# Performance work log

Hardware: AMD Instinct MI355X
Metric: run time of the kernel (lower is better)

Reference implementation:

```python
import jax, jax.numpy as jnp
import numpy as np

B, S, D, H = 4096, 200, 64, 36
BN_EPS = 1e-5
DICE_EPS = 1e-3


def setup_inputs() -> dict:
    key = jax.random.key(0)
    ks = jax.random.split(key, 6)
    return {
        "history": jax.random.normal(ks[0], (B, S, D), dtype=jnp.float32),
        "candidate": jax.random.normal(ks[1], (B, D), dtype=jnp.float32),
        "W1": jax.random.normal(ks[2], (4 * D, H), dtype=jnp.float32) * 0.05,
        "b1": jax.random.normal(ks[3], (H,), dtype=jnp.float32) * 0.05,
        "gamma": jnp.ones((H,), dtype=jnp.float32),
        "beta": jnp.zeros((H,), dtype=jnp.float32),
        "alpha": jax.random.normal(ks[4], (1,), dtype=jnp.float32),
        "W2": jax.random.normal(ks[5], (H, 1), dtype=jnp.float32) * 0.05,
        "b2": jnp.zeros((1,), dtype=jnp.float32),
    }


def reference(history, candidate, W1, b1, gamma, beta, alpha, W2, b2):
    b, s, d = history.shape
    cand = jnp.broadcast_to(candidate[:, None, :], (b, s, d))
    att_in = jnp.concatenate([cand, history, cand - history, cand * history], axis=-1)
    x = att_in.reshape(b * s, 4 * d)
    # Linear
    h = x @ W1 + b1
    # BatchNorm1d (training mode: batch statistics, biased variance)
    mu = h.mean(axis=0)
    var = h.var(axis=0)
    h = (h - mu) * jax.lax.rsqrt(var + BN_EPS) * gamma + beta
    # Dice: per-row normalization over features, eps=1e-3
    avg = h.mean(axis=1, keepdims=True)
    v = jnp.sum((h - avg) ** 2, axis=1, keepdims=True) / h.shape[1]
    ps = jax.nn.sigmoid((h - avg) / jnp.sqrt(v + DICE_EPS))
    h = ps * h + (1.0 - ps) * alpha * h
    # Output linear -> attention weight per (b, s)
    w = (h @ W2 + b2).reshape(b, s)
    # Weighted sum pooling over sequence
    return jnp.einsum("bs,bsd->bd", w, history)
```

## Files before the change

kernel.cpp:

```cpp
#include <hip/hip_runtime.h>
#include <math.h>

#define BB 4096
#define SS 200
#define DD 64
#define HH 36
#define NP 48
#define NROWS (BB * SS)
#define LDH 72
#define MT 13

typedef short bf16x8 __attribute__((ext_vector_type(8)));
typedef float f32x4 __attribute__((ext_vector_type(4)));

__device__ __forceinline__ unsigned short f2bf(float f) {
    union { float f; unsigned u; } v; v.f = f;
    unsigned r = v.u + 0x7FFFu + ((v.u >> 16) & 1u);
    return (unsigned short)(r >> 16);
}

__device__ __forceinline__ void build_tiles(int b, int t,
                                            const float* __restrict__ hist,
                                            const float* __restrict__ cand,
                                            const float* __restrict__ W1,
                                            const float* __restrict__ b1,
                                            unsigned short* shH, unsigned short* shWbT,
                                            float* shC, float* shBase,
                                            float (*shBaseP)[NP]) {
    if (t < DD) shC[t] = cand[b * DD + t];
    for (int i = t; i < 8 * DD; i += 256) {
        int s = SS + (i >> 6), d = i & 63;
        shH[s * LDH + d] = 0;
    }
    __syncthreads();
    const float4* src = (const float4*)(hist + (size_t)b * (SS * DD));
    for (int i = t; i < SS * DD / 4; i += 256) {
        float4 v = src[i];
        int s = i >> 4, c = i & 15;
        ushort4 o;
        o.x = f2bf(v.x); o.y = f2bf(v.y); o.z = f2bf(v.z); o.w = f2bf(v.w);
        *(ushort4*)&shH[s * LDH + c * 4] = o;
    }
    for (int e = t; e < NP * DD; e += 256) {
        int k = e / NP, n = e - k * NP;
        float v = 0.f;
        if (n < HH)
            v = W1[(DD + k) * HH + n] - W1[(2 * DD + k) * HH + n] +
                shC[k] * W1[(3 * DD + k) * HH + n];
        shWbT[n * LDH + k] = f2bf(v);
    }
    if (t < 4 * NP) {
        int g = t / NP, j = t - g * NP;
        float p = 0.f;
        if (j < HH) {
#pragma unroll 4
            for (int k = 16 * g; k < 16 * g + 16; ++k)
                p += shC[k] * (W1[k * HH + j] + W1[(2 * DD + k) * HH + j]);
        }
        shBaseP[g][j] = p;
    }
    __syncthreads();
    if (t < NP) {
        float v = (t < HH) ? b1[t] : 0.f;
        shBase[t] = v + shBaseP[0][t] + shBaseP[1][t] + shBaseP[2][t] + shBaseP[3][t];
    }
    __syncthreads();
}

__device__ __forceinline__ void load_bfrags(const unsigned short* shWbT, int lane,
                                            bf16x8 (&bfr)[3][2]) {
    int col = lane & 15, q = lane >> 4;
#pragma unroll
    for (int nt = 0; nt < 3; ++nt)
#pragma unroll
        for (int kt = 0; kt < 2; ++kt)
            bfr[nt][kt] = *(const bf16x8*)&shWbT[(nt * 16 + col) * LDH + kt * 32 + q * 8];
}

__device__ __forceinline__ void gemm_tile(const unsigned short* shH,
                                          const bf16x8 (&bfr)[3][2], int mt, int lane,
                                          f32x4 (&d)[3]) {
    int m = mt * 16 + (lane & 15), q = lane >> 4;
    d[0] = f32x4{0.f, 0.f, 0.f, 0.f};
    d[1] = f32x4{0.f, 0.f, 0.f, 0.f};
    d[2] = f32x4{0.f, 0.f, 0.f, 0.f};
#pragma unroll
    for (int kt = 0; kt < 2; ++kt) {
        bf16x8 a = *(const bf16x8*)&shH[m * LDH + kt * 32 + q * 8];
#pragma unroll
        for (int nt = 0; nt < 3; ++nt)
            d[nt] = __builtin_amdgcn_mfma_f32_16x16x32_bf16(a, bfr[nt][kt], d[nt], 0, 0, 0);
    }
}

__global__ __launch_bounds__(256, 4) void k_pass1(const float* __restrict__ hist,
                                                  const float* __restrict__ cand,
                                                  const float* __restrict__ W1,
                                                  const float* __restrict__ b1,
                                                  float* __restrict__ gsum,
                                                  float* __restrict__ gsum2) {
    __shared__ unsigned short shH[208 * LDH];
    __shared__ unsigned short shWbT[NP * LDH];
    __shared__ float shC[DD], shBase[NP];
    __shared__ float shBaseP[4][NP];
    __shared__ float shP1[4][NP], shP2[4][NP];
    int b = blockIdx.x, t = threadIdx.x, wave = t >> 6, lane = t & 63;
    int col = lane & 15, q = lane >> 4;

    build_tiles(b, t, hist, cand, W1, b1, shH, shWbT, shC, shBase, shBaseP);

    bf16x8 bfr[3][2];
    load_bfrags(shWbT, lane, bfr);
    float basev[3];
#pragma unroll
    for (int nt = 0; nt < 3; ++nt) basev[nt] = shBase[nt * 16 + col];

    float cs1[3] = {0.f, 0.f, 0.f}, cs2[3] = {0.f, 0.f, 0.f};
    for (int mt = wave; mt < MT; mt += 4) {
        f32x4 d[3];
        gemm_tile(shH, bfr, mt, lane, d);
        int row0 = mt * 16 + q * 4;
#pragma unroll
        for (int nt = 0; nt < 3; ++nt)
#pragma unroll
            for (int r = 0; r < 4; ++r) {
                if (row0 + r < SS) {
                    float v = d[nt][r] + basev[nt];
                    cs1[nt] += v;
                    cs2[nt] += v * v;
                }
            }
    }
#pragma unroll
    for (int nt = 0; nt < 3; ++nt) {
        cs1[nt] += __shfl_xor(cs1[nt], 16);
        cs1[nt] += __shfl_xor(cs1[nt], 32);
        cs2[nt] += __shfl_xor(cs2[nt], 16);
        cs2[nt] += __shfl_xor(cs2[nt], 32);
    }
    if (lane < 16) {
#pragma unroll
        for (int nt = 0; nt < 3; ++nt) {
            shP1[wave][nt * 16 + lane] = cs1[nt];
            shP2[wave][nt * 16 + lane] = cs2[nt];
        }
    }
    __syncthreads();
    if (t < HH) {
        atomicAdd(gsum + t, shP1[0][t] + shP1[1][t] + shP1[2][t] + shP1[3][t]);
        atomicAdd(gsum2 + t, shP2[0][t] + shP2[1][t] + shP2[2][t] + shP2[3][t]);
    }
}

__global__ void k_stats(const float* __restrict__ gsum, const float* __restrict__ gsum2,
                        const float* __restrict__ gamma, const float* __restrict__ beta,
                        float* __restrict__ A, float* __restrict__ Bc) {
    int t = threadIdx.x;
    if (t < NP) {
        if (t < HH) {
            float mu = gsum[t] * (1.0f / (float)NROWS);
            float var = gsum2[t] * (1.0f / (float)NROWS) - mu * mu;
            float rs = rsqrtf(var + 1e-5f);
            float a = rs * gamma[t];
            A[t] = a;
            Bc[t] = beta[t] - mu * a;
        } else {
            A[t] = 0.f;
            Bc[t] = 0.f;
        }
    }
}

__global__ __launch_bounds__(256, 4) void k_pass2(const float* __restrict__ hist,
                                                  const float* __restrict__ cand,
                                                  const float* __restrict__ W1,
                                                  const float* __restrict__ b1,
                                                  const float* __restrict__ Acoef,
                                                  const float* __restrict__ Bcoef,
                                                  const float* __restrict__ alpha,
                                                  const float* __restrict__ W2,
                                                  const float* __restrict__ b2,
                                                  float* __restrict__ out) {
    __shared__ unsigned short shH[208 * LDH];
    __shared__ unsigned short shWbT[NP * LDH];
    __shared__ float shC[DD], shBase[NP];
    __shared__ float shBaseP[4][NP];
    __shared__ float shW[208];
    __shared__ float shPool[4][DD];
    int b = blockIdx.x, t = threadIdx.x, wave = t >> 6, lane = t & 63;
    int col = lane & 15, q = lane >> 4;

    build_tiles(b, t, hist, cand, W1, b1, shH, shWbT, shC, shBase, shBaseP);

    bf16x8 bfr[3][2];
    load_bfrags(shWbT, lane, bfr);
    float basev[3], Ar[3], Br[3], W2r[3];
#pragma unroll
    for (int nt = 0; nt < 3; ++nt) {
        int c = nt * 16 + col;
        basev[nt] = shBase[c];
        Ar[nt] = Acoef[c];
        Br[nt] = Bcoef[c];
        W2r[nt] = (c < HH) ? W2[c] : 0.f;
    }
    float alv = alpha[0], b2v = b2[0];

    for (int mt = wave; mt < MT; mt += 4) {
        f32x4 d[3];
        gemm_tile(shH, bfr, mt, lane, d);
        float hp[3][4];
#pragma unroll
        for (int nt = 0; nt < 3; ++nt)
#pragma unroll
            for (int r = 0; r < 4; ++r)
                hp[nt][r] = fmaf(d[nt][r] + basev[nt], Ar[nt], Br[nt]);
        float s1[4], s2[4], wsum[4];
#pragma unroll
        for (int r = 0; r < 4; ++r) {
            s1[r] = hp[0][r] + hp[1][r] + hp[2][r];
            s2[r] = hp[0][r] * hp[0][r] + hp[1][r] * hp[1][r] + hp[2][r] * hp[2][r];
            s1[r] += __shfl_xor(s1[r], 1);
            s1[r] += __shfl_xor(s1[r], 2);
            s1[r] += __shfl_xor(s1[r], 4);
            s1[r] += __shfl_xor(s1[r], 8);
            s2[r] += __shfl_xor(s2[r], 1);
            s2[r] += __shfl_xor(s2[r], 2);
            s2[r] += __shfl_xor(s2[r], 4);
            s2[r] += __shfl_xor(s2[r], 8);
        }
#pragma unroll
        for (int r = 0; r < 4; ++r) {
            float avg = s1[r] * (1.0f / (float)HH);
            float var = s2[r] * (1.0f / (float)HH) - avg * avg;
            float inv = rsqrtf(var + 1e-3f);
            float wv = 0.f;
#pragma unroll
            for (int nt = 0; nt < 3; ++nt) {
                float z = (hp[nt][r] - avg) * inv;
                float ps = 1.0f / (1.0f + __expf(-z));
                float f = ps + (1.0f - ps) * alv;
                wv = fmaf(hp[nt][r] * f, W2r[nt], wv);
            }
            wsum[r] = wv;
            wsum[r] += __shfl_xor(wsum[r], 1);
            wsum[r] += __shfl_xor(wsum[r], 2);
            wsum[r] += __shfl_xor(wsum[r], 4);
            wsum[r] += __shfl_xor(wsum[r], 8);
        }
        if (col == 0 && !(mt == MT - 1 && q >= 2)) {
            float4 o = {wsum[0] + b2v, wsum[1] + b2v, wsum[2] + b2v, wsum[3] + b2v};
            *(float4*)&shW[mt * 16 + q * 4] = o;
        }
    }
    __syncthreads();
    {
        const float* hb = hist + (size_t)b * SS * DD;
        float p = 0.f;
        int s0 = wave * 50;
        for (int s = s0; s < s0 + 50; ++s) p = fmaf(shW[s], hb[(size_t)s * DD + lane], p);
        shPool[wave][lane] = p;
    }
    __syncthreads();
    if (t < DD)
        out[b * DD + t] = shPool[0][t] + shPool[1][t] + shPool[2][t] + shPool[3][t];
}

extern "C" void kernel_launch(void* const* d_in, const int* in_sizes, int n_in,
                              void* d_out, int out_size, void* d_ws, size_t ws_size,
                              hipStream_t stream) {
    const float* hist = (const float*)d_in[0];
    const float* cand = (const float*)d_in[1];
    const float* W1 = (const float*)d_in[2];
    const float* b1 = (const float*)d_in[3];
    const float* gamma = (const float*)d_in[4];
    const float* beta = (const float*)d_in[5];
    const float* alpha = (const float*)d_in[6];
    const float* W2 = (const float*)d_in[7];
    const float* b2 = (const float*)d_in[8];
    float* out = (float*)d_out;
    float* ws = (float*)d_ws;

    float* gsum = ws;
    float* gsum2 = ws + NP;
    float* A = ws + 2 * NP;
    float* Bc = ws + 3 * NP;

    hipMemsetAsync(gsum, 0, 2 * NP * sizeof(float), stream);
    k_pass1<<<BB, 256, 0, stream>>>(hist, cand, W1, b1, gsum, gsum2);
    k_stats<<<1, 64, 0, stream>>>(gsum, gsum2, gamma, beta, A, Bc);
    k_pass2<<<BB, 256, 0, stream>>>(hist, cand, W1, b1, A, Bc, alpha, W2, b2, out);
}
```

Baseline: 475.4 us.

## Split each batch row across two blocks with smaller LDS tiles

Each batch element is now handled by two blocks, one for rows 0-111 and one for rows 112-199, which doubles the grid and roughly halves the shared-memory footprint per block. Launch bounds rise to 6 blocks per CU and the LDS stride shrinks to 68. History loads are issued into registers before the first barrier so more memory traffic is in flight. Pooled outputs are combined with atomicAdd after a memset of the output buffer. In exchange, the candidate and weight prologue is computed twice per batch row, and the new atomics and memset add their own cost.

Result: slower. 591.5 us (+24.4%).

```diff
diff --git a/kernel.cpp b/kernel.cpp
--- a/kernel.cpp
+++ b/kernel.cpp
@@ -6,9 +6,8 @@
 #define DD 64
 #define HH 36
 #define NP 48
-#define NROWS (BB * SS)
-#define LDH 72
-#define MT 13
+#define LDH 68
+#define NROWSF (4096.0f * 200.0f)
 
 typedef short bf16x8 __attribute__((ext_vector_type(8)));
 typedef float f32x4 __attribute__((ext_vector_type(4)));
@@ -19,35 +18,46 @@
     return (unsigned short)(r >> 16);
 }
 
-__device__ __forceinline__ void build_tiles(int b, int t,
-                                            const float* __restrict__ hist,
-                                            const float* __restrict__ cand,
-                                            const float* __restrict__ W1,
-                                            const float* __restrict__ b1,
-                                            unsigned short* shH, unsigned short* shWbT,
-                                            float* shC, float* shBase,
-                                            float (*shBaseP)[NP]) {
+__device__ __forceinline__ void prologue(int b, int half, int t,
+                                         const float* __restrict__ hist,
+                                         const float* __restrict__ cand,
+                                         const float* __restrict__ W1,
+                                         const float* __restrict__ b1,
+                                         unsigned short* shH, unsigned short* shWbT,
+                                         float* shC, float* shBase,
+                                         float (*shBaseP)[NP]) {
+    const int rowLo = half ? 112 : 0;
+    const int nflt4 = half ? (88 * 16) : (112 * 16);
+    float4 v[7];
+    const float4* src = (const float4*)(hist + ((size_t)b * SS + rowLo) * DD);
+#pragma unroll
+    for (int u = 0; u < 7; ++u) {
+        int i = t + u * 256;
+        if (i < nflt4) v[u] = src[i];
+    }
     if (t < DD) shC[t] = cand[b * DD + t];
-    for (int i = t; i < 8 * DD; i += 256) {
-        int s = SS + (i >> 6), d = i & 63;
-        shH[s * LDH + d] = 0;
-    }
-    __syncthreads();
-    const float4* src = (const float4*)(hist + (size_t)b * (SS * DD));
-    for (int i = t; i < SS * DD / 4; i += 256) {
-        float4 v = src[i];
-        int s = i >> 4, c = i & 15;
-        ushort4 o;
-        o.x = f2bf(v.x); o.y = f2bf(v.y); o.z = f2bf(v.z); o.w = f2bf(v.w);
-        *(ushort4*)&shH[s * LDH + c * 4] = o;
+    if (half) {
+        for (int i = t; i < 8 * DD; i += 256)
+            shH[(88 + (i >> 6)) * LDH + (i & 63)] = 0;
+    }
+    __syncthreads();
+#pragma unroll
+    for (int u = 0; u < 7; ++u) {
+        int i = t + u * 256;
+        if (i < nflt4) {
+            int s = i >> 4, c = i & 15;
+            ushort4 o;
+            o.x = f2bf(v[u].x); o.y = f2bf(v[u].y); o.z = f2bf(v[u].z); o.w = f2bf(v[u].w);
+            *(ushort4*)&shH[s * LDH + c * 4] = o;
+        }
     }
     for (int e = t; e < NP * DD; e += 256) {
         int k = e / NP, n = e - k * NP;
-        float v = 0.f;
+        float val = 0.f;
         if (n < HH)
-            v = W1[(DD + k) * HH + n] - W1[(2 * DD + k) * HH + n] +
-                shC[k] * W1[(3 * DD + k) * HH + n];
-        shWbT[n * LDH + k] = f2bf(v);
+            val = W1[(DD + k) * HH + n] - W1[(2 * DD + k) * HH + n] +
+                  shC[k] * W1[(3 * DD + k) * HH + n];
+        shWbT[n * LDH + k] = f2bf(val);
     }
     if (t < 4 * NP) {
         int g = t / NP, j = t - g * NP;
@@ -61,8 +71,8 @@
     }
     __syncthreads();
     if (t < NP) {
-        float v = (t < HH) ? b1[t] : 0.f;
-        shBase[t] = v + shBaseP[0][t] + shBaseP[1][t] + shBaseP[2][t] + shBaseP[3][t];
+        float val = (t < HH) ? b1[t] : 0.f;
+        shBase[t] = val + shBaseP[0][t] + shBaseP[1][t] + shBaseP[2][t] + shBaseP[3][t];
     }
     __syncthreads();
 }
@@ -93,21 +103,22 @@
     }
 }
 
-__global__ __launch_bounds__(256, 4) void k_pass1(const float* __restrict__ hist,
+__global__ __launch_bounds__(256, 6) void k_pass1(const float* __restrict__ hist,
                                                   const float* __restrict__ cand,
                                                   const float* __restrict__ W1,
                                                   const float* __restrict__ b1,
                                                   float* __restrict__ gsum,
                                                   float* __restrict__ gsum2) {
-    __shared__ unsigned short shH[208 * LDH];
+    __shared__ unsigned short shH[112 * LDH];
     __shared__ unsigned short shWbT[NP * LDH];
     __shared__ float shC[DD], shBase[NP];
     __shared__ float shBaseP[4][NP];
     __shared__ float shP1[4][NP], shP2[4][NP];
-    int b = blockIdx.x, t = threadIdx.x, wave = t >> 6, lane = t & 63;
+    int bx = blockIdx.x, b = bx >> 1, half = bx & 1;
+    int t = threadIdx.x, wave = t >> 6, lane = t & 63;
     int col = lane & 15, q = lane >> 4;
 
-    build_tiles(b, t, hist, cand, W1, b1, shH, shWbT, shC, shBase, shBaseP);
+    prologue(b, half, t, hist, cand, W1, b1, shH, shWbT, shC, shBase, shBaseP);
 
     bf16x8 bfr[3][2];
     load_bfrags(shWbT, lane, bfr);
@@ -115,19 +126,20 @@
 #pragma unroll
     for (int nt = 0; nt < 3; ++nt) basev[nt] = shBase[nt * 16 + col];
 
+    const int T0 = half ? 7 : 0, NTl = half ? 6 : 7;
     float cs1[3] = {0.f, 0.f, 0.f}, cs2[3] = {0.f, 0.f, 0.f};
-    for (int mt = wave; mt < MT; mt += 4) {
+    for (int mt = wave; mt < NTl; mt += 4) {
         f32x4 d[3];
         gemm_tile(shH, bfr, mt, lane, d);
-        int row0 = mt * 16 + q * 4;
+        int grow0 = (T0 + mt) * 16 + q * 4;
 #pragma unroll
         for (int nt = 0; nt < 3; ++nt)
 #pragma unroll
             for (int r = 0; r < 4; ++r) {
-                if (row0 + r < SS) {
-                    float v = d[nt][r] + basev[nt];
-                    cs1[nt] += v;
-                    cs2[nt] += v * v;
+                if (grow0 + r < SS) {
+                    float vv = d[nt][r] + basev[nt];
+                    cs1[nt] += vv;
+                    cs2[nt] += vv * vv;
                 }
             }
     }
@@ -158,8 +170,8 @@
     int t = threadIdx.x;
     if (t < NP) {
         if (t < HH) {
-            float mu = gsum[t] * (1.0f / (float)NROWS);
-            float var = gsum2[t] * (1.0f / (float)NROWS) - mu * mu;
+            float mu = gsum[t] * (1.0f / NROWSF);
+            float var = gsum2[t] * (1.0f / NROWSF) - mu * mu;
             float rs = rsqrtf(var + 1e-5f);
             float a = rs * gamma[t];
             A[t] = a;
@@ -171,7 +183,7 @@
     }
 }
 
-__global__ __launch_bounds__(256, 4) void k_pass2(const float* __restrict__ hist,
+__global__ __launch_bounds__(256, 6) void k_pass2(const float* __restrict__ hist,
                                                   const float* __restrict__ cand,
                                                   const float* __restrict__ W1,
                                                   const float* __restrict__ b1,
@@ -181,16 +193,17 @@
                                                   const float* __restrict__ W2,
                                                   const float* __restrict__ b2,
                                                   float* __restrict__ out) {
-    __shared__ unsigned short shH[208 * LDH];
+    __shared__ unsigned short shH[112 * LDH];
     __shared__ unsigned short shWbT[NP * LDH];
     __shared__ float shC[DD], shBase[NP];
     __shared__ float shBaseP[4][NP];
-    __shared__ float shW[208];
+    __shared__ float shW[112];
     __shared__ float shPool[4][DD];
-    int b = blockIdx.x, t = threadIdx.x, wave = t >> 6, lane = t & 63;
+    int bx = blockIdx.x, b = bx >> 1, half = bx & 1;
+    int t = threadIdx.x, wave = t >> 6, lane = t & 63;
     int col = lane & 15, q = lane >> 4;
 
-    build_tiles(b, t, hist, cand, W1, b1, shH, shWbT, shC, shBase, shBaseP);
+    prologue(b, half, t, hist, cand, W1, b1, shH, shWbT, shC, shBase, shBaseP);
 
     bf16x8 bfr[3][2];
     load_bfrags(shWbT, lane, bfr);
@@ -205,7 +218,8 @@
     }
     float alv = alpha[0], b2v = b2[0];
 
-    for (int mt = wave; mt < MT; mt += 4) {
+    const int T0 = half ? 7 : 0, NTl = half ? 6 : 7;
+    for (int mt = wave; mt < NTl; mt += 4) {
         f32x4 d[3];
         gemm_tile(shH, bfr, mt, lane, d);
         float hp[3][4];
@@ -247,22 +261,25 @@
             wsum[r] += __shfl_xor(wsum[r], 4);
             wsum[r] += __shfl_xor(wsum[r], 8);
         }
-        if (col == 0 && !(mt == MT - 1 && q >= 2)) {
+        int grow0 = (T0 + mt) * 16 + q * 4;
+        if (col == 0 && grow0 + 3 < SS) {
             float4 o = {wsum[0] + b2v, wsum[1] + b2v, wsum[2] + b2v, wsum[3] + b2v};
             *(float4*)&shW[mt * 16 + q * 4] = o;
         }
     }
     __syncthreads();
     {
+        const int rowLo = T0 * 16, nR = half ? 88 : 112;
         const float* hb = hist + (size_t)b * SS * DD;
         float p = 0.f;
-        int s0 = wave * 50;
-        for (int s = s0; s < s0 + 50; ++s) p = fmaf(shW[s], hb[(size_t)s * DD + lane], p);
+        for (int s = wave; s < nR; s += 4)
+            p = fmaf(shW[s], hb[(size_t)(rowLo + s) * DD + lane], p);
         shPool[wave][lane] = p;
     }
     __syncthreads();
     if (t < DD)
-        out[b * DD + t] = shPool[0][t] + shPool[1][t] + shPool[2][t] + shPool[3][t];
+        atomicAdd(out + b * DD + t,
+                  shPool[0][t] + shPool[1][t] + shPool[2][t] + shPool[3][t]);
 }
 
 extern "C" void kernel_launch(void* const* d_in, const int* in_sizes, int n_in,
@@ -286,7 +303,8 @@
     float* Bc = ws + 3 * NP;
 
     hipMemsetAsync(gsum, 0, 2 * NP * sizeof(float), stream);
-    k_pass1<<<BB, 256, 0, stream>>>(hist, cand, W1, b1, gsum, gsum2);
+    hipMemsetAsync(out, 0, (size_t)out_size * sizeof(float), stream);
+    k_pass1<<<2 * BB, 256, 0, stream>>>(hist, cand, W1, b1, gsum, gsum2);
     k_stats<<<1, 64, 0, stream>>>(gsum, gsum2, gamma, beta, A, Bc);
-    k_pass2<<<BB, 256, 0, stream>>>(hist, cand, W1, b1, A, Bc, alpha, W2, b2, out);
-}
+    k_pass2<<<2 * BB, 256, 0, stream>>>(hist, cand, W1, b1, A, Bc, alpha, W2, b2, out);
+}
```
